# Performance work log

Hardware: AMD Instinct MI355X
Metric: run time of the kernel (lower is better)

The kernel has to match this reference:

```python
import jax, jax.numpy as jnp
import numpy as np

D_MODEL = 1024
D_STATE = 16  # hardcoded in original: A = randn(d_model, 16)


def setup_inputs() -> dict:
    key = jax.random.key(0)
    ks = jax.random.split(key, 9)
    D = D_MODEL
    s = 1.0 / np.sqrt(D)
    x = jax.random.normal(ks[0], (4, 8192, D), dtype=jnp.float32)
    in_w = jax.random.uniform(ks[1], (2 * D, D), minval=-s, maxval=s, dtype=jnp.float32)
    in_b = jax.random.uniform(ks[2], (2 * D,), minval=-s, maxval=s, dtype=jnp.float32)
    out_w = jax.random.uniform(ks[3], (D, D), minval=-s, maxval=s, dtype=jnp.float32)
    out_b = jax.random.uniform(ks[4], (D,), minval=-s, maxval=s, dtype=jnp.float32)
    dt_w = jax.random.uniform(ks[5], (D, D), minval=-s, maxval=s, dtype=jnp.float32)
    dt_b = jax.random.uniform(ks[6], (D,), minval=-s, maxval=s, dtype=jnp.float32)
    A = jax.random.normal(ks[7], (D, D_STATE), dtype=jnp.float32)
    Dp = jax.random.normal(ks[8], (D,), dtype=jnp.float32)
    return {"x": x, "in_w": in_w, "in_b": in_b, "out_w": out_w, "out_b": out_b,
            "dt_w": dt_w, "dt_b": dt_b, "A": A, "Dp": Dp}


def reference(x, in_w, in_b, out_w, out_b, dt_w, dt_b, A, Dp):
    # x: [B, L, D]. in_proj -> [B, L, 2D], split into x_val / res.
    x_and_res = jnp.einsum('bld,ed->ble', x, in_w) + in_b
    x_val, res = jnp.split(x_and_res, 2, axis=-1)
    # Original computes dt = softplus(dt_proj(xt)) per timestep but never uses it
    # (dead compute, A/Dp/h also unused); output depends only on silu gating.
    # y_t = xt * sigmoid(xt) == silu(x_val), fully parallel over L (no recurrence).
    y = x_val * jax.nn.sigmoid(x_val)
    gated = y * jax.nn.silu(res)
    return jnp.einsum('bld,ed->ble', gated, out_w) + out_b
```

## Files before the change

### kernel.cpp

```cpp
#include <hip/hip_runtime.h>
#include <cstdint>


typedef __bf16 bf16x8 __attribute__((ext_vector_type(8)));
typedef float f32x16 __attribute__((ext_vector_type(16)));

#define KD 1024
#define BUF_ELEMS 16384

__device__ __forceinline__ void gload_lds16(const void* g, void* lds_u) {
  __builtin_amdgcn_global_load_lds(
      (__attribute__((address_space(1))) void*)(uintptr_t)g,
      (__attribute__((address_space(3))) void*)(uint32_t)(uintptr_t)lds_u,
      16, 0, 0);
}

#define WAITB(N) do { \
  asm volatile("s_waitcnt vmcnt(" #N ")" ::: "memory"); \
  asm volatile("s_barrier" ::: "memory"); } while (0)

__global__ void cast_all(const float* __restrict__ x, __bf16* __restrict__ xb,
                         const float* __restrict__ in_w, __bf16* __restrict__ w1b,
                         const float* __restrict__ out_w, __bf16* __restrict__ w2b) {
  const int b = blockIdx.x;
  if (b < 16384) {
    int i = b * 256 + threadIdx.x;
    const float4* p = (const float4*)x;
    float4 v0 = p[2 * i];
    float4 v1 = p[2 * i + 1];
    bf16x8 o;
    o[0] = (__bf16)v0.x; o[1] = (__bf16)v0.y; o[2] = (__bf16)v0.z; o[3] = (__bf16)v0.w;
    o[4] = (__bf16)v1.x; o[5] = (__bf16)v1.y; o[6] = (__bf16)v1.z; o[7] = (__bf16)v1.w;
    ((bf16x8*)xb)[i] = o;
  } else if (b < 17408) {
    int i = (b - 16384) * 256 + threadIdx.x;
    int orow = i >> 7;
    int chunk = i & 127;
    int bb = orow >> 5, t = orow & 31;
    int srow = (bb & 1) * 1024 + (bb >> 1) * 32 + t;
    const float4* p = (const float4*)(in_w + ((size_t)srow << 10) + (chunk << 3));
    float4 v0 = p[0], v1 = p[1];
    bf16x8 o;
    o[0] = (__bf16)v0.x; o[1] = (__bf16)v0.y; o[2] = (__bf16)v0.z; o[3] = (__bf16)v0.w;
    o[4] = (__bf16)v1.x; o[5] = (__bf16)v1.y; o[6] = (__bf16)v1.z; o[7] = (__bf16)v1.w;
    *(bf16x8*)(w1b + ((size_t)orow << 10) + (chunk << 3)) = o;
  } else {
    int i = (b - 17408) * 256 + threadIdx.x;
    const float4* p = (const float4*)out_w;
    float4 v0 = p[2 * i];
    float4 v1 = p[2 * i + 1];
    bf16x8 o;
    o[0] = (__bf16)v0.x; o[1] = (__bf16)v0.y; o[2] = (__bf16)v0.z; o[3] = (__bf16)v0.w;
    o[4] = (__bf16)v1.x; o[5] = (__bf16)v1.y; o[6] = (__bf16)v1.z; o[7] = (__bf16)v1.w;
    ((bf16x8*)w2b)[i] = o;
  }
}

template <int BUF>
__device__ __forceinline__ void stage_tile(const __bf16*& pa, const __bf16*& pb,
                                           __bf16* smw) {
  __bf16* d = smw + BUF * BUF_ELEMS;
  gload_lds16(pa, d);
  gload_lds16(pa + 128 * KD, d + 4096);
  gload_lds16(pb, d + 8192);
  gload_lds16(pb + 128 * KD, d + 12288);
  pa += 32;
  pb += 32;
}

template <int BUF>
__device__ __forceinline__ void compute_tile(const __bf16* sm,
                                             int aRow, int bRow,
                                             int o0, int o1,
                                             f32x16 (&acc)[4][2]) {
  const __bf16* base = sm + BUF * BUF_ELEMS;
  bf16x8 a0[4], a1[4], b0[2], b1[2];
  b0[0] = *(const bf16x8*)(base + bRow + o0);
  b1[0] = *(const bf16x8*)(base + bRow + o1);
  b0[1] = *(const bf16x8*)(base + bRow + 1024 + o1);
  b1[1] = *(const bf16x8*)(base + bRow + 1024 + o0);
#pragma unroll
  for (int i = 0; i < 4; ++i) {
    const int e0 = (i & 1) ? o1 : o0;
    const int e1 = (i & 1) ? o0 : o1;
    a0[i] = *(const bf16x8*)(base + aRow + i * 1024 + e0);
    a1[i] = *(const bf16x8*)(base + aRow + i * 1024 + e1);
  }
  __builtin_amdgcn_s_setprio(1);
#pragma unroll
  for (int i = 0; i < 4; ++i)
#pragma unroll
    for (int j = 0; j < 2; ++j)
      acc[i][j] = __builtin_amdgcn_mfma_f32_32x32x16_bf16(a0[i], b0[j], acc[i][j], 0, 0, 0);
#pragma unroll
  for (int i = 0; i < 4; ++i)
#pragma unroll
    for (int j = 0; j < 2; ++j)
      acc[i][j] = __builtin_amdgcn_mfma_f32_32x32x16_bf16(a1[i], b1[j], acc[i][j], 0, 0, 0);
  __builtin_amdgcn_s_setprio(0);
}

__device__ __forceinline__ void gemm_core(const __bf16* __restrict__ A,
                                          const __bf16* __restrict__ B,
                                          __bf16* sm, long m0, long n0,
                                          f32x16 (&acc)[4][2]) {
  const int t = threadIdx.x;
  const int w = t >> 6;
  const int lane = t & 63;
  const int c31 = lane & 31;
  const int hi = lane >> 5;
  const int wr = w >> 2;
  const int wc = w & 3;

  const int l = lane;
  const int stg_row = w * 16 + (l >> 2);
  const int stg_col = ((l & 3) ^ ((l >> 3) & 3) ^ (w & 3)) << 3;
  const __bf16* pa = A + (m0 + stg_row) * KD + stg_col;
  const __bf16* pb = B + (n0 + stg_row) * KD + stg_col;
  __bf16* smw = sm + w * 512;

  const int key_base = ((c31 >> 1) & 3) ^ ((c31 >> 4) & 1);
  const int o0 = (hi ^ key_base) << 3;
  const int o1 = o0 ^ 16;
  const int aRow = (wr * 128 + c31) * 32;
  const int bRow = 8192 + (wc * 64 + c31) * 32;

#pragma unroll
  for (int i = 0; i < 4; ++i)
#pragma unroll
    for (int j = 0; j < 2; ++j)
      acc[i][j] = (f32x16){0.f, 0.f, 0.f, 0.f, 0.f, 0.f, 0.f, 0.f,
                           0.f, 0.f, 0.f, 0.f, 0.f, 0.f, 0.f, 0.f};

  stage_tile<0>(pa, pb, smw);
  stage_tile<1>(pa, pb, smw);

  for (int it = 0; it < 10; ++it) {
    WAITB(4); stage_tile<2>(pa, pb, smw);
    compute_tile<0>(sm, aRow, bRow, o0, o1, acc);
    WAITB(4); stage_tile<0>(pa, pb, smw);
    compute_tile<1>(sm, aRow, bRow, o0, o1, acc);
    WAITB(4); stage_tile<1>(pa, pb, smw);
    compute_tile<2>(sm, aRow, bRow, o0, o1, acc);
  }
  WAITB(4); compute_tile<0>(sm, aRow, bRow, o0, o1, acc);
  WAITB(0); compute_tile<1>(sm, aRow, bRow, o0, o1, acc);
}

__global__ __launch_bounds__(512, 2)
void gemm1_silu(const __bf16* __restrict__ X, const __bf16* __restrict__ W1i,
                const float* __restrict__ in_b, __bf16* __restrict__ G) {
  __shared__ __bf16 sm[3 * BUF_ELEMS];
  const int bid = blockIdx.x;
  const int swz = (bid & 7) * 128 + (bid >> 3);
  const long m0 = (long)(swz >> 3) * 256;
  const long n0 = (long)(swz & 7) * 256;

  f32x16 acc[4][2];
  gemm_core(X, W1i, sm, m0, n0, acc);

  const int lane = threadIdx.x & 63;
  const int w = threadIdx.x >> 6;
  const int wr = w >> 2, wc = w & 3;
  const int c31 = lane & 31;
  const int hi = lane >> 5;

  const int gc = ((int)n0 >> 1) + wc * 32 + c31;
  const float bx = in_b[gc];
  const float br = in_b[1024 + gc];

#pragma unroll
  for (int i = 0; i < 4; ++i)
#pragma unroll
    for (int reg = 0; reg < 16; ++reg) {
      const int row = wr * 128 + i * 32 + (reg & 3) + 8 * (reg >> 2) + 4 * hi;
      float xv = acc[i][0][reg] + bx;
      float rs = acc[i][1][reg] + br;
      float e1 = __expf(-xv);
      float e2 = __expf(-rs);
      float g = xv * rs * __builtin_amdgcn_rcpf((1.0f + e1) * (1.0f + e2));
      G[(m0 + row) * 1024 + gc] = (__bf16)g;
    }
}

__global__ __launch_bounds__(512, 2)
void gemm2_bias(const __bf16* __restrict__ G, const __bf16* __restrict__ W2,
                const float* __restrict__ out_b, float* __restrict__ OUT) {
  __shared__ __bf16 sm[3 * BUF_ELEMS];
  const int bid = blockIdx.x;
  const int swz = (bid & 7) * 64 + (bid >> 3);
  const long m0 = (long)(swz >> 2) * 256;
  const long n0 = (long)(swz & 3) * 256;

  f32x16 acc[4][2];
  gemm_core(G, W2, sm, m0, n0, acc);

  const int lane = threadIdx.x & 63;
  const int w = threadIdx.x >> 6;
  const int wr = w >> 2, wc = w & 3;
  const int c31 = lane & 31;
  const int hi = lane >> 5;

  float ob[2];
#pragma unroll
  for (int j = 0; j < 2; ++j)
    ob[j] = out_b[(int)n0 + wc * 64 + j * 32 + c31];
#pragma unroll
  for (int i = 0; i < 4; ++i)
#pragma unroll
    for (int j = 0; j < 2; ++j)
#pragma unroll
      for (int reg = 0; reg < 16; ++reg) {
        const int row = wr * 128 + i * 32 + (reg & 3) + 8 * (reg >> 2) + 4 * hi;
        const int col = (int)n0 + wc * 64 + j * 32 + c31;
        OUT[(m0 + row) * 1024 + col] = acc[i][j][reg] + ob[j];
      }
}

extern "C" void kernel_launch(void* const* d_in, const int* in_sizes, int n_in,
                              void* d_out, int out_size, void* d_ws, size_t ws_size,
                              hipStream_t stream) {
  const float* x = (const float*)d_in[0];
  const float* in_w = (const float*)d_in[1];
  const float* in_b = (const float*)d_in[2];
  const float* out_w = (const float*)d_in[3];
  const float* out_b = (const float*)d_in[4];

  char* ws = (char*)d_ws;
  __bf16* xb = (__bf16*)(ws);
  __bf16* w1b = (__bf16*)(ws + (size_t)67108864);
  __bf16* w2b = (__bf16*)(ws + (size_t)71303168);
  __bf16* gb = (__bf16*)(ws + (size_t)73400320);

  cast_all<<<dim3(17920), 256, 0, stream>>>(x, xb, in_w, w1b, out_w, w2b);
  gemm1_silu<<<dim3(1024), 512, 0, stream>>>(xb, w1b, in_b, gb);
  gemm2_bias<<<dim3(512), 512, 0, stream>>>(gb, w2b, out_b, (float*)d_out);
}
```

Before: 261.4 us.

## Fuse fp32-to-bf16 activation cast into gemm1 A-tile staging

Drops the separate pass that cast the full x tensor to bf16. gemm1 now loads fp32 x into registers, converts it, and writes bf16 into LDS with the same swizzle, while B keeps using direct global-to-LDS loads. This removes a large read/write round trip of the activation through HBM and one kernel's worth of traffic. In exchange the A path goes through registers with extra VGPR pressure, ds_write traffic and lgkmcnt waits, and each gemm1 block reads fp32 x twice as wide, reloaded across the 8 N-tiles.

```diff
diff --git a/kernel.cpp b/kernel.cpp
--- a/kernel.cpp
+++ b/kernel.cpp
@@ -19,21 +19,17 @@
   asm volatile("s_waitcnt vmcnt(" #N ")" ::: "memory"); \
   asm volatile("s_barrier" ::: "memory"); } while (0)
 
-__global__ void cast_all(const float* __restrict__ x, __bf16* __restrict__ xb,
-                         const float* __restrict__ in_w, __bf16* __restrict__ w1b,
-                         const float* __restrict__ out_w, __bf16* __restrict__ w2b) {
+#define WAITBL(N) do { \
+  asm volatile("s_waitcnt vmcnt(" #N ") lgkmcnt(0)" ::: "memory"); \
+  asm volatile("s_barrier" ::: "memory"); } while (0)
+
+#define FENCE asm volatile("" ::: "memory")
+
+__global__ void cast_weights(const float* __restrict__ in_w, __bf16* __restrict__ w1b,
+                             const float* __restrict__ out_w, __bf16* __restrict__ w2b) {
   const int b = blockIdx.x;
-  if (b < 16384) {
+  if (b < 1024) {
     int i = b * 256 + threadIdx.x;
-    const float4* p = (const float4*)x;
-    float4 v0 = p[2 * i];
-    float4 v1 = p[2 * i + 1];
-    bf16x8 o;
-    o[0] = (__bf16)v0.x; o[1] = (__bf16)v0.y; o[2] = (__bf16)v0.z; o[3] = (__bf16)v0.w;
-    o[4] = (__bf16)v1.x; o[5] = (__bf16)v1.y; o[6] = (__bf16)v1.z; o[7] = (__bf16)v1.w;
-    ((bf16x8*)xb)[i] = o;
-  } else if (b < 17408) {
-    int i = (b - 16384) * 256 + threadIdx.x;
     int orow = i >> 7;
     int chunk = i & 127;
     int bb = orow >> 5, t = orow & 31;
@@ -45,7 +41,7 @@
     o[4] = (__bf16)v1.x; o[5] = (__bf16)v1.y; o[6] = (__bf16)v1.z; o[7] = (__bf16)v1.w;
     *(bf16x8*)(w1b + ((size_t)orow << 10) + (chunk << 3)) = o;
   } else {
-    int i = (b - 17408) * 256 + threadIdx.x;
+    int i = (b - 1024) * 256 + threadIdx.x;
     const float4* p = (const float4*)out_w;
     float4 v0 = p[2 * i];
     float4 v1 = p[2 * i + 1];
@@ -57,15 +53,38 @@
 }
 
 template <int BUF>
-__device__ __forceinline__ void stage_tile(const __bf16*& pa, const __bf16*& pb,
-                                           __bf16* smw) {
-  __bf16* d = smw + BUF * BUF_ELEMS;
+__device__ __forceinline__ void stageB(const __bf16*& pb, __bf16* smwB) {
+  __bf16* d = smwB + BUF * BUF_ELEMS;
+  gload_lds16(pb, d);
+  gload_lds16(pb + 128 * KD, d + 4096);
+  pb += 32;
+}
+
+template <int BUF>
+__device__ __forceinline__ void stageA_g(const __bf16*& pa, __bf16* smwA) {
+  __bf16* d = smwA + BUF * BUF_ELEMS;
   gload_lds16(pa, d);
   gload_lds16(pa + 128 * KD, d + 4096);
-  gload_lds16(pb, d + 8192);
-  gload_lds16(pb + 128 * KD, d + 12288);
   pa += 32;
-  pb += 32;
+}
+
+__device__ __forceinline__ void ldA(float4 (&r)[4], const float* p) {
+  r[0] = *(const float4*)p;
+  r[1] = *(const float4*)(p + 4);
+  r[2] = *(const float4*)(p + 128 * 1024);
+  r[3] = *(const float4*)(p + 128 * 1024 + 4);
+}
+
+template <int BUF>
+__device__ __forceinline__ void dswrA(const float4 (&r)[4], __bf16* dwA) {
+  __bf16* d = dwA + BUF * BUF_ELEMS;
+  bf16x8 lo, hi;
+  lo[0] = (__bf16)r[0].x; lo[1] = (__bf16)r[0].y; lo[2] = (__bf16)r[0].z; lo[3] = (__bf16)r[0].w;
+  lo[4] = (__bf16)r[1].x; lo[5] = (__bf16)r[1].y; lo[6] = (__bf16)r[1].z; lo[7] = (__bf16)r[1].w;
+  hi[0] = (__bf16)r[2].x; hi[1] = (__bf16)r[2].y; hi[2] = (__bf16)r[2].z; hi[3] = (__bf16)r[2].w;
+  hi[4] = (__bf16)r[3].x; hi[5] = (__bf16)r[3].y; hi[6] = (__bf16)r[3].z; hi[7] = (__bf16)r[3].w;
+  *(bf16x8*)d = lo;
+  *(bf16x8*)(d + 4096) = hi;
 }
 
 template <int BUF>
@@ -100,6 +119,78 @@
   __builtin_amdgcn_s_setprio(0);
 }
 
+__device__ __forceinline__ void gemm1_core(const float* __restrict__ X32,
+                                           const __bf16* __restrict__ B,
+                                           __bf16* sm, long m0, long n0,
+                                           f32x16 (&acc)[4][2]) {
+  const int t = threadIdx.x;
+  const int w = t >> 6;
+  const int lane = t & 63;
+  const int c31 = lane & 31;
+  const int hi = lane >> 5;
+  const int wr = w >> 2;
+  const int wc = w & 3;
+  const int l = lane;
+
+  const int stg_row = w * 16 + (l >> 2);
+  const int stg_col = ((l & 3) ^ ((l >> 3) & 3) ^ (w & 3)) << 3;
+  const __bf16* pb = B + (n0 + stg_row) * KD + stg_col;
+  __bf16* smwB = sm + 8192 + w * 512;
+
+  const float* pxk = X32 + (m0 + stg_row) * 1024 + (l & 3) * 8;
+  const int aphys = (l & 3) ^ ((l >> 3) & 3) ^ (w & 3);
+  __bf16* dwA = sm + stg_row * 32 + aphys * 8;
+
+  const int key_base = ((c31 >> 1) & 3) ^ ((c31 >> 4) & 1);
+  const int o0 = (hi ^ key_base) << 3;
+  const int o1 = o0 ^ 16;
+  const int aRow = (wr * 128 + c31) * 32;
+  const int bRow = 8192 + (wc * 64 + c31) * 32;
+
+#pragma unroll
+  for (int i = 0; i < 4; ++i)
+#pragma unroll
+    for (int j = 0; j < 2; ++j)
+      acc[i][j] = (f32x16){0.f, 0.f, 0.f, 0.f, 0.f, 0.f, 0.f, 0.f,
+                           0.f, 0.f, 0.f, 0.f, 0.f, 0.f, 0.f, 0.f};
+
+  float4 rA[4];
+  ldA(rA, pxk); pxk += 32;
+  FENCE;
+  stageB<0>(pb, smwB);
+  asm volatile("s_waitcnt vmcnt(2)" ::: "memory");
+  dswrA<0>(rA, dwA);
+  ldA(rA, pxk); pxk += 32;
+  FENCE;
+  stageB<1>(pb, smwB);
+
+  for (int it = 0; it < 10; ++it) {
+    WAITBL(2);
+    dswrA<1>(rA, dwA);
+    ldA(rA, pxk); pxk += 32;
+    FENCE;
+    stageB<2>(pb, smwB);
+    compute_tile<0>(sm, aRow, bRow, o0, o1, acc);
+    WAITBL(2);
+    dswrA<2>(rA, dwA);
+    ldA(rA, pxk); pxk += 32;
+    FENCE;
+    stageB<0>(pb, smwB);
+    compute_tile<1>(sm, aRow, bRow, o0, o1, acc);
+    WAITBL(2);
+    dswrA<0>(rA, dwA);
+    ldA(rA, pxk); pxk += 32;
+    FENCE;
+    stageB<1>(pb, smwB);
+    compute_tile<2>(sm, aRow, bRow, o0, o1, acc);
+  }
+  WAITBL(2);
+  dswrA<1>(rA, dwA);
+  compute_tile<0>(sm, aRow, bRow, o0, o1, acc);
+  WAITBL(0);
+  compute_tile<1>(sm, aRow, bRow, o0, o1, acc);
+}
+
 __device__ __forceinline__ void gemm_core(const __bf16* __restrict__ A,
                                           const __bf16* __restrict__ B,
                                           __bf16* sm, long m0, long n0,
@@ -111,13 +202,14 @@
   const int hi = lane >> 5;
   const int wr = w >> 2;
   const int wc = w & 3;
-
   const int l = lane;
+
   const int stg_row = w * 16 + (l >> 2);
   const int stg_col = ((l & 3) ^ ((l >> 3) & 3) ^ (w & 3)) << 3;
   const __bf16* pa = A + (m0 + stg_row) * KD + stg_col;
   const __bf16* pb = B + (n0 + stg_row) * KD + stg_col;
-  __bf16* smw = sm + w * 512;
+  __bf16* smwA = sm + w * 512;
+  __bf16* smwB = sm + 8192 + w * 512;
 
   const int key_base = ((c31 >> 1) & 3) ^ ((c31 >> 4) & 1);
   const int o0 = (hi ^ key_base) << 3;
@@ -132,15 +224,15 @@
       acc[i][j] = (f32x16){0.f, 0.f, 0.f, 0.f, 0.f, 0.f, 0.f, 0.f,
                            0.f, 0.f, 0.f, 0.f, 0.f, 0.f, 0.f, 0.f};
 
-  stage_tile<0>(pa, pb, smw);
-  stage_tile<1>(pa, pb, smw);
+  stageA_g<0>(pa, smwA); stageB<0>(pb, smwB);
+  stageA_g<1>(pa, smwA); stageB<1>(pb, smwB);
 
   for (int it = 0; it < 10; ++it) {
-    WAITB(4); stage_tile<2>(pa, pb, smw);
+    WAITB(4); stageA_g<2>(pa, smwA); stageB<2>(pb, smwB);
     compute_tile<0>(sm, aRow, bRow, o0, o1, acc);
-    WAITB(4); stage_tile<0>(pa, pb, smw);
+    WAITB(4); stageA_g<0>(pa, smwA); stageB<0>(pb, smwB);
     compute_tile<1>(sm, aRow, bRow, o0, o1, acc);
-    WAITB(4); stage_tile<1>(pa, pb, smw);
+    WAITB(4); stageA_g<1>(pa, smwA); stageB<1>(pb, smwB);
     compute_tile<2>(sm, aRow, bRow, o0, o1, acc);
   }
   WAITB(4); compute_tile<0>(sm, aRow, bRow, o0, o1, acc);
@@ -148,7 +240,7 @@
 }
 
 __global__ __launch_bounds__(512, 2)
-void gemm1_silu(const __bf16* __restrict__ X, const __bf16* __restrict__ W1i,
+void gemm1_silu(const float* __restrict__ X32, const __bf16* __restrict__ W1i,
                 const float* __restrict__ in_b, __bf16* __restrict__ G) {
   __shared__ __bf16 sm[3 * BUF_ELEMS];
   const int bid = blockIdx.x;
@@ -157,7 +249,7 @@
   const long n0 = (long)(swz & 7) * 256;
 
   f32x16 acc[4][2];
-  gemm_core(X, W1i, sm, m0, n0, acc);
+  gemm1_core(X32, W1i, sm, m0, n0, acc);
 
   const int lane = threadIdx.x & 63;
   const int w = threadIdx.x >> 6;
@@ -227,12 +319,11 @@
   const float* out_b = (const float*)d_in[4];
 
   char* ws = (char*)d_ws;
-  __bf16* xb = (__bf16*)(ws);
-  __bf16* w1b = (__bf16*)(ws + (size_t)67108864);
-  __bf16* w2b = (__bf16*)(ws + (size_t)71303168);
-  __bf16* gb = (__bf16*)(ws + (size_t)73400320);
-
-  cast_all<<<dim3(17920), 256, 0, stream>>>(x, xb, in_w, w1b, out_w, w2b);
-  gemm1_silu<<<dim3(1024), 512, 0, stream>>>(xb, w1b, in_b, gb);
+  __bf16* w1b = (__bf16*)(ws);
+  __bf16* w2b = (__bf16*)(ws + (size_t)4194304);
+  __bf16* gb = (__bf16*)(ws + (size_t)6291456);
+
+  cast_weights<<<dim3(1536), 256, 0, stream>>>(in_w, w1b, out_w, w2b);
+  gemm1_silu<<<dim3(1024), 512, 0, stream>>>(x, w1b, in_b, gb);
   gemm2_bias<<<dim3(512), 512, 0, stream>>>(gb, w2b, out_b, (float*)d_out);
 }
```

After: 332.0 us. 1.27x slower.

## Load B operand directly from global into registers, stage only A in LDS

Applied to the files above, without the earlier changes.

B-operand fragments are now loaded straight from global memory into registers with a double-buffered register set, and only the A tile is staged through LDS. The A pipeline goes from three to four LDS buffers. This removes LDS write/read traffic and capacity for B, and allows deeper prefetch of A. In exchange it adds register pressure, and each wave loads its B fragments from global memory itself. With four waves sharing each B slice that is redundant traffic through the caches, and it relies on the vmcnt wait counts staying correct.

```diff
diff --git a/kernel.cpp b/kernel.cpp
--- a/kernel.cpp
+++ b/kernel.cpp
@@ -6,7 +6,7 @@
 typedef float f32x16 __attribute__((ext_vector_type(16)));
 
 #define KD 1024
-#define BUF_ELEMS 16384
+#define ABUF_ELEMS 8192
 
 __device__ __forceinline__ void gload_lds16(const void* g, void* lds_u) {
   __builtin_amdgcn_global_load_lds(
@@ -57,48 +57,38 @@
 }
 
 template <int BUF>
-__device__ __forceinline__ void stage_tile(const __bf16*& pa, const __bf16*& pb,
-                                           __bf16* smw) {
-  __bf16* d = smw + BUF * BUF_ELEMS;
+__device__ __forceinline__ void stageA(const __bf16*& pa, __bf16* smw) {
+  __bf16* d = smw + BUF * ABUF_ELEMS;
   gload_lds16(pa, d);
   gload_lds16(pa + 128 * KD, d + 4096);
-  gload_lds16(pb, d + 8192);
-  gload_lds16(pb + 128 * KD, d + 12288);
   pa += 32;
-  pb += 32;
-}
-
-template <int BUF>
-__device__ __forceinline__ void compute_tile(const __bf16* sm,
-                                             int aRow, int bRow,
-                                             int o0, int o1,
-                                             f32x16 (&acc)[4][2]) {
-  const __bf16* base = sm + BUF * BUF_ELEMS;
-  bf16x8 a0[4], a1[4], b0[2], b1[2];
-  b0[0] = *(const bf16x8*)(base + bRow + o0);
-  b1[0] = *(const bf16x8*)(base + bRow + o1);
-  b0[1] = *(const bf16x8*)(base + bRow + 1024 + o1);
-  b1[1] = *(const bf16x8*)(base + bRow + 1024 + o0);
-#pragma unroll
-  for (int i = 0; i < 4; ++i) {
-    const int e0 = (i & 1) ? o1 : o0;
-    const int e1 = (i & 1) ? o0 : o1;
-    a0[i] = *(const bf16x8*)(base + aRow + i * 1024 + e0);
-    a1[i] = *(const bf16x8*)(base + aRow + i * 1024 + e1);
-  }
-  __builtin_amdgcn_s_setprio(1);
-#pragma unroll
-  for (int i = 0; i < 4; ++i)
-#pragma unroll
-    for (int j = 0; j < 2; ++j)
-      acc[i][j] = __builtin_amdgcn_mfma_f32_32x32x16_bf16(a0[i], b0[j], acc[i][j], 0, 0, 0);
-#pragma unroll
-  for (int i = 0; i < 4; ++i)
-#pragma unroll
-    for (int j = 0; j < 2; ++j)
-      acc[i][j] = __builtin_amdgcn_mfma_f32_32x32x16_bf16(a1[i], b1[j], acc[i][j], 0, 0, 0);
-  __builtin_amdgcn_s_setprio(0);
-}
+}
+
+#define LDB(SET) do { \
+  SET[0][0] = *(const bf16x8*)(pb0); \
+  SET[0][1] = *(const bf16x8*)(pb0 + 16); \
+  SET[1][0] = *(const bf16x8*)(pb1); \
+  SET[1][1] = *(const bf16x8*)(pb1 + 16); \
+  pb0 += 32; pb1 += 32; \
+} while (0)
+
+#define CTILE(BUF, SET) do { \
+  const __bf16* base_ = sm + (BUF) * ABUF_ELEMS; \
+  bf16x8 a0[4], a1[4]; \
+  _Pragma("unroll") for (int i = 0; i < 4; ++i) { \
+    const int e0 = (i & 1) ? o1 : o0; \
+    a0[i] = *(const bf16x8*)(base_ + aRow + i * 1024 + e0); \
+    a1[i] = *(const bf16x8*)(base_ + aRow + i * 1024 + (e0 ^ 16)); \
+  } \
+  __builtin_amdgcn_s_setprio(1); \
+  _Pragma("unroll") for (int i = 0; i < 4; ++i) \
+    _Pragma("unroll") for (int j = 0; j < 2; ++j) \
+      acc[i][j] = __builtin_amdgcn_mfma_f32_32x32x16_bf16(a0[i], SET[j][0], acc[i][j], 0, 0, 0); \
+  _Pragma("unroll") for (int i = 0; i < 4; ++i) \
+    _Pragma("unroll") for (int j = 0; j < 2; ++j) \
+      acc[i][j] = __builtin_amdgcn_mfma_f32_32x32x16_bf16(a1[i], SET[j][1], acc[i][j], 0, 0, 0); \
+  __builtin_amdgcn_s_setprio(0); \
+} while (0)
 
 __device__ __forceinline__ void gemm_core(const __bf16* __restrict__ A,
                                           const __bf16* __restrict__ B,
@@ -116,14 +106,17 @@
   const int stg_row = w * 16 + (l >> 2);
   const int stg_col = ((l & 3) ^ ((l >> 3) & 3) ^ (w & 3)) << 3;
   const __bf16* pa = A + (m0 + stg_row) * KD + stg_col;
-  const __bf16* pb = B + (n0 + stg_row) * KD + stg_col;
   __bf16* smw = sm + w * 512;
+
+  const __bf16* pb0 = B + (n0 + wc * 64 + c31) * KD + hi * 8;
+  const __bf16* pb1 = pb0 + 32 * KD;
 
   const int key_base = ((c31 >> 1) & 3) ^ ((c31 >> 4) & 1);
   const int o0 = (hi ^ key_base) << 3;
   const int o1 = o0 ^ 16;
   const int aRow = (wr * 128 + c31) * 32;
-  const int bRow = 8192 + (wc * 64 + c31) * 32;
+
+  bf16x8 bfP[2][2], bfQ[2][2];
 
 #pragma unroll
   for (int i = 0; i < 4; ++i)
@@ -132,25 +125,27 @@
       acc[i][j] = (f32x16){0.f, 0.f, 0.f, 0.f, 0.f, 0.f, 0.f, 0.f,
                            0.f, 0.f, 0.f, 0.f, 0.f, 0.f, 0.f, 0.f};
 
-  stage_tile<0>(pa, pb, smw);
-  stage_tile<1>(pa, pb, smw);
-
-  for (int it = 0; it < 10; ++it) {
-    WAITB(4); stage_tile<2>(pa, pb, smw);
-    compute_tile<0>(sm, aRow, bRow, o0, o1, acc);
-    WAITB(4); stage_tile<0>(pa, pb, smw);
-    compute_tile<1>(sm, aRow, bRow, o0, o1, acc);
-    WAITB(4); stage_tile<1>(pa, pb, smw);
-    compute_tile<2>(sm, aRow, bRow, o0, o1, acc);
+  stageA<0>(pa, smw);
+  LDB(bfP);
+  stageA<1>(pa, smw);
+  WAITB(2);
+
+  for (int it = 0; it < 7; ++it) {
+    LDB(bfQ); stageA<2>(pa, smw); CTILE(0, bfP); WAITB(2);
+    LDB(bfP); stageA<3>(pa, smw); CTILE(1, bfQ); WAITB(2);
+    LDB(bfQ); stageA<0>(pa, smw); CTILE(2, bfP); WAITB(2);
+    LDB(bfP); stageA<1>(pa, smw); CTILE(3, bfQ); WAITB(2);
   }
-  WAITB(4); compute_tile<0>(sm, aRow, bRow, o0, o1, acc);
-  WAITB(0); compute_tile<1>(sm, aRow, bRow, o0, o1, acc);
+  LDB(bfQ); stageA<2>(pa, smw); CTILE(0, bfP); WAITB(2);
+  LDB(bfP); stageA<3>(pa, smw); CTILE(1, bfQ); WAITB(2);
+  LDB(bfQ);                      CTILE(2, bfP); WAITB(0);
+  CTILE(3, bfQ);
 }
 
 __global__ __launch_bounds__(512, 2)
 void gemm1_silu(const __bf16* __restrict__ X, const __bf16* __restrict__ W1i,
                 const float* __restrict__ in_b, __bf16* __restrict__ G) {
-  __shared__ __bf16 sm[3 * BUF_ELEMS];
+  __shared__ __bf16 sm[4 * ABUF_ELEMS];
   const int bid = blockIdx.x;
   const int swz = (bid & 7) * 128 + (bid >> 3);
   const long m0 = (long)(swz >> 3) * 256;
@@ -186,7 +181,7 @@
 __global__ __launch_bounds__(512, 2)
 void gemm2_bias(const __bf16* __restrict__ G, const __bf16* __restrict__ W2,
                 const float* __restrict__ out_b, float* __restrict__ OUT) {
-  __shared__ __bf16 sm[3 * BUF_ELEMS];
+  __shared__ __bf16 sm[4 * ABUF_ELEMS];
   const int bid = blockIdx.x;
   const int swz = (bid & 7) * 64 + (bid >> 3);
   const long m0 = (long)(swz >> 2) * 256;
```

After: 337.0 us. 1.29x slower.

## Split each K-tile into two barrier-gated phases interleaving LDS reads, stages, and MFMAs

Applied to the files above, without the earlier changes.

Restructures the main GEMM loop so each K-tile is computed in two half-phases. Each phase loads its own A/B fragments from LDS and issues half of the next tile's global-to-LDS copies, then passes a barrier plus lgkmcnt wait before its MFMA burst at raised priority. This is meant to spread memory issue across the compute and keep waves in lockstep so LDS reads and MFMAs overlap better, and it halves register pressure for fragments. The cost is two extra workgroup barriers per tile, which can stall waves.

```diff
diff --git a/kernel.cpp b/kernel.cpp
--- a/kernel.cpp
+++ b/kernel.cpp
@@ -18,6 +18,12 @@
 #define WAITB(N) do { \
   asm volatile("s_waitcnt vmcnt(" #N ")" ::: "memory"); \
   asm volatile("s_barrier" ::: "memory"); } while (0)
+
+#define PH_GATE() do { \
+  __builtin_amdgcn_s_barrier(); \
+  asm volatile("s_waitcnt lgkmcnt(0)" ::: "memory"); \
+  __builtin_amdgcn_sched_barrier(0); \
+  __builtin_amdgcn_s_setprio(1); } while (0)
 
 __global__ void cast_all(const float* __restrict__ x, __bf16* __restrict__ xb,
                          const float* __restrict__ in_w, __bf16* __restrict__ w1b,
@@ -56,6 +62,53 @@
   }
 }
 
+template <int BUF, int SBUF, bool DO_STAGE>
+__device__ __forceinline__ void compute_tile(const __bf16* sm,
+                                             int aRow, int bRow,
+                                             int o0, int o1,
+                                             const __bf16*& pa, const __bf16*& pb,
+                                             __bf16* smw,
+                                             f32x16 (&acc)[4][2]) {
+  const __bf16* base = sm + BUF * BUF_ELEMS;
+  __bf16* d = smw + SBUF * BUF_ELEMS;
+  bf16x8 a0[4], b0[2];
+  b0[0] = *(const bf16x8*)(base + bRow + o0);
+  b0[1] = *(const bf16x8*)(base + bRow + 1024 + o1);
+#pragma unroll
+  for (int i = 0; i < 4; ++i)
+    a0[i] = *(const bf16x8*)(base + aRow + i * 1024 + ((i & 1) ? o1 : o0));
+  if (DO_STAGE) {
+    gload_lds16(pa, d);
+    gload_lds16(pa + 128 * KD, d + 4096);
+    pa += 32;
+  }
+  PH_GATE();
+#pragma unroll
+  for (int i = 0; i < 4; ++i)
+#pragma unroll
+    for (int j = 0; j < 2; ++j)
+      acc[i][j] = __builtin_amdgcn_mfma_f32_32x32x16_bf16(a0[i], b0[j], acc[i][j], 0, 0, 0);
+  __builtin_amdgcn_s_setprio(0);
+  bf16x8 a1[4], b1[2];
+  b1[0] = *(const bf16x8*)(base + bRow + o1);
+  b1[1] = *(const bf16x8*)(base + bRow + 1024 + o0);
+#pragma unroll
+  for (int i = 0; i < 4; ++i)
+    a1[i] = *(const bf16x8*)(base + aRow + i * 1024 + ((i & 1) ? o0 : o1));
+  if (DO_STAGE) {
+    gload_lds16(pb, d + 8192);
+    gload_lds16(pb + 128 * KD, d + 12288);
+    pb += 32;
+  }
+  PH_GATE();
+#pragma unroll
+  for (int i = 0; i < 4; ++i)
+#pragma unroll
+    for (int j = 0; j < 2; ++j)
+      acc[i][j] = __builtin_amdgcn_mfma_f32_32x32x16_bf16(a1[i], b1[j], acc[i][j], 0, 0, 0);
+  __builtin_amdgcn_s_setprio(0);
+}
+
 template <int BUF>
 __device__ __forceinline__ void stage_tile(const __bf16*& pa, const __bf16*& pb,
                                            __bf16* smw) {
@@ -66,38 +119,6 @@
   gload_lds16(pb + 128 * KD, d + 12288);
   pa += 32;
   pb += 32;
-}
-
-template <int BUF>
-__device__ __forceinline__ void compute_tile(const __bf16* sm,
-                                             int aRow, int bRow,
-                                             int o0, int o1,
-                                             f32x16 (&acc)[4][2]) {
-  const __bf16* base = sm + BUF * BUF_ELEMS;
-  bf16x8 a0[4], a1[4], b0[2], b1[2];
-  b0[0] = *(const bf16x8*)(base + bRow + o0);
-  b1[0] = *(const bf16x8*)(base + bRow + o1);
-  b0[1] = *(const bf16x8*)(base + bRow + 1024 + o1);
-  b1[1] = *(const bf16x8*)(base + bRow + 1024 + o0);
-#pragma unroll
-  for (int i = 0; i < 4; ++i) {
-    const int e0 = (i & 1) ? o1 : o0;
-    const int e1 = (i & 1) ? o0 : o1;
-    a0[i] = *(const bf16x8*)(base + aRow + i * 1024 + e0);
-    a1[i] = *(const bf16x8*)(base + aRow + i * 1024 + e1);
-  }
-  __builtin_amdgcn_s_setprio(1);
-#pragma unroll
-  for (int i = 0; i < 4; ++i)
-#pragma unroll
-    for (int j = 0; j < 2; ++j)
-      acc[i][j] = __builtin_amdgcn_mfma_f32_32x32x16_bf16(a0[i], b0[j], acc[i][j], 0, 0, 0);
-#pragma unroll
-  for (int i = 0; i < 4; ++i)
-#pragma unroll
-    for (int j = 0; j < 2; ++j)
-      acc[i][j] = __builtin_amdgcn_mfma_f32_32x32x16_bf16(a1[i], b1[j], acc[i][j], 0, 0, 0);
-  __builtin_amdgcn_s_setprio(0);
 }
 
 __device__ __forceinline__ void gemm_core(const __bf16* __restrict__ A,
@@ -136,15 +157,17 @@
   stage_tile<1>(pa, pb, smw);
 
   for (int it = 0; it < 10; ++it) {
-    WAITB(4); stage_tile<2>(pa, pb, smw);
-    compute_tile<0>(sm, aRow, bRow, o0, o1, acc);
-    WAITB(4); stage_tile<0>(pa, pb, smw);
-    compute_tile<1>(sm, aRow, bRow, o0, o1, acc);
-    WAITB(4); stage_tile<1>(pa, pb, smw);
-    compute_tile<2>(sm, aRow, bRow, o0, o1, acc);
-  }
-  WAITB(4); compute_tile<0>(sm, aRow, bRow, o0, o1, acc);
-  WAITB(0); compute_tile<1>(sm, aRow, bRow, o0, o1, acc);
+    WAITB(4);
+    compute_tile<0, 2, true>(sm, aRow, bRow, o0, o1, pa, pb, smw, acc);
+    WAITB(4);
+    compute_tile<1, 0, true>(sm, aRow, bRow, o0, o1, pa, pb, smw, acc);
+    WAITB(4);
+    compute_tile<2, 1, true>(sm, aRow, bRow, o0, o1, pa, pb, smw, acc);
+  }
+  WAITB(4);
+  compute_tile<0, 2, false>(sm, aRow, bRow, o0, o1, pa, pb, smw, acc);
+  WAITB(0);
+  compute_tile<1, 2, false>(sm, aRow, bRow, o0, o1, pa, pb, smw, acc);
 }
 
 __global__ __launch_bounds__(512, 2)
```

New measurement: 252.9 us, median of 2. 3.2% less time.
